# Kernel tuning notes

Measured on AMD Instinct MI355X. Metric: run time of the kernel, lower is better.

The kernel has to match this reference:

```python
import jax, jax.numpy as jnp
import numpy as np

B, S, D, H = 2, 2048, 1024, 16
HD = D // H  # 64


def setup_inputs() -> dict:
    key = jax.random.key(0)
    ks = jax.random.split(key, 10)
    sc = 1.0 / np.sqrt(D)
    return {
        "decoder_hs": jax.random.normal(ks[0], (B, S, D), jnp.float32),
        "encoder_hs": jax.random.normal(ks[1], (B, S, D), jnp.float32),
        "Wq": jax.random.normal(ks[2], (D, D), jnp.float32) * sc,
        "bq": jax.random.normal(ks[3], (D,), jnp.float32) * 0.02,
        "Wk": jax.random.normal(ks[4], (D, D), jnp.float32) * sc,
        "bk": jax.random.normal(ks[5], (D,), jnp.float32) * 0.02,
        "Wv": jax.random.normal(ks[6], (D, D), jnp.float32) * sc,
        "bv": jax.random.normal(ks[7], (D,), jnp.float32) * 0.02,
        "Wp": jax.random.normal(ks[8], (D, D), jnp.float32) * sc,
        "bp": jax.random.normal(ks[9], (D,), jnp.float32) * 0.02,
    }


def reference(decoder_hs, encoder_hs, Wq, bq, Wk, bk, Wv, bv, Wp, bp):
    b, s, d = decoder_hs.shape
    # torch nn.Linear: y = x @ W.T + b, W is [out, in]
    q = decoder_hs @ Wq.T + bq
    k = encoder_hs @ Wk.T + bk
    v = encoder_hs @ Wv.T + bv
    # head split: [b, s, d] -> [b, h, s, hd]
    q = q.reshape(b, s, H, HD).transpose(0, 2, 1, 3)
    k = k.reshape(b, s, H, HD).transpose(0, 2, 1, 3)
    v = v.reshape(b, s, H, HD).transpose(0, 2, 1, 3)
    scale = 1.0 / np.sqrt(HD).astype(np.float32)
    att = jnp.einsum('bhqd,bhkd->bhqk', q, k) * scale
    att = jax.nn.softmax(att, axis=-1)
    y = jnp.einsum('bhqk,bhkd->bhqd', att, v)
    y = y.transpose(0, 2, 1, 3).reshape(b, s, d)
    return y @ Wp.T + bp
```

## Files before the change

kernel.cpp:

```cpp
#include <hip/hip_runtime.h>
#include <hip/hip_bf16.h>
#include <cstdint>
#include <cstddef>

#define BB 2
#define SS 2048
#define DD 1024
#define HH 16
#define HD 64

typedef __attribute__((ext_vector_type(8))) short bf16x8;
typedef __attribute__((ext_vector_type(4))) short bf16x4;
typedef __attribute__((ext_vector_type(4))) float f32x4;

#define MFMA16(va, vb, c) __builtin_amdgcn_mfma_f32_16x16x16bf16_1k(va, vb, c, 0, 0, 0)

#define GLL(g, l) __builtin_amdgcn_global_load_lds( \
    (const __attribute__((address_space(1))) void*)(g), \
    (__attribute__((address_space(3))) void*)(l), 16, 0, 0)

__device__ __forceinline__ short f2bf_fast(float f) {
    uint32_t u = __float_as_uint(f);
    u += 0x7FFF + ((u >> 16) & 1);
    return (short)(u >> 16);
}
__device__ __forceinline__ uint32_t pack_bf2(float a, float b) {
    uint32_t ua = __float_as_uint(a), ub = __float_as_uint(b);
    ua += 0x7FFF + ((ua >> 16) & 1);
    ub += 0x7FFF + ((ub >> 16) & 1);
    return (ua >> 16) | (ub & 0xFFFF0000u);
}
__device__ __forceinline__ bf16x8 cvt8(const float* __restrict__ p) {
    float4 a = *(const float4*)p;
    float4 b = *(const float4*)(p + 4);
    union { uint32_t d[4]; bf16x8 v; } r;
    r.d[0] = pack_bf2(a.x, a.y);
    r.d[1] = pack_bf2(a.z, a.w);
    r.d[2] = pack_bf2(b.x, b.y);
    r.d[3] = pack_bf2(b.z, b.w);
    return r.v;
}

__global__ __launch_bounds__(256) void cvt6_kernel(
    const float* __restrict__ s0, const float* __restrict__ s1,
    const float* __restrict__ s2, const float* __restrict__ s3,
    const float* __restrict__ s4, const float* __restrict__ s5,
    short* __restrict__ d0, short* __restrict__ d1, short* __restrict__ d2,
    short* __restrict__ d3, short* __restrict__ d4, short* __restrict__ d5)
{
    const int z = blockIdx.z;
    const float* s = (z == 0) ? s0 : (z == 1) ? s1 : (z == 2) ? s2
                   : (z == 3) ? s3 : (z == 4) ? s4 : s5;
    short* d = (z == 0) ? d0 : (z == 1) ? d1 : (z == 2) ? d2
             : (z == 3) ? d3 : (z == 4) ? d4 : d5;
    const int n8 = (z < 2) ? (BB * SS * DD / 8) : (DD * DD / 8);
    const int id = blockIdx.x * 256 + threadIdx.x;
    if (id >= n8) return;
    bf16x8 r = cvt8(s + (size_t)id * 8);
    *(uint4*)(d + (size_t)id * 8) = *(uint4*)&r;
}

template<int BF>
__global__ __launch_bounds__(256, 3) void qkv_gemm_kernel(
    const void* __restrict__ dec, const void* __restrict__ enc,
    const void* __restrict__ Wq, const void* __restrict__ Wk,
    const void* __restrict__ Wv,
    const float* __restrict__ bq, const float* __restrict__ bk,
    const float* __restrict__ bv,
    short* __restrict__ Qo, short* __restrict__ Ko, short* __restrict__ Vo)
{
    __shared__ short As[128 * 32];
    __shared__ short Bs[128 * 32];

    const int z = blockIdx.z;
    const void* Xv = (z == 0) ? dec : enc;
    const void* Wp_ = (z == 0) ? Wq : (z == 1) ? Wk : Wv;
    const float* bias = (z == 0) ? bq : (z == 1) ? bk : bv;
    short* Yo = (z == 0) ? Qo : (z == 1) ? Ko : Vo;

    const int t = threadIdx.x;
    const int lane = t & 63, wv = t >> 6;
    const int lr = lane & 15, quad = lane >> 4;
    const int wm = wv >> 1, wn = wv & 1;
    const int m0 = blockIdx.y * 128;
    const int n0 = blockIdx.x * 128;
    const int K = DD;

    f32x4 acc[4][4];
    #pragma unroll
    for (int i = 0; i < 4; i++)
        #pragma unroll
        for (int j = 0; j < 4; j++) acc[i][j] = (f32x4){0.f, 0.f, 0.f, 0.f};

    for (int kb = 0; kb < K; kb += 32) {
        __syncthreads();
        if (BF) {
            const short* Xb = (const short*)Xv;
            const short* Wb = (const short*)Wp_;
            #pragma unroll
            for (int c = 0; c < 2; c++) {
                int r0 = wv * 32 + c * 16;
                int r = r0 + (lane >> 2), ch = (lane & 3) * 8;
                GLL(Xb + (size_t)(m0 + r) * K + kb + ch, &As[r0 * 32]);
                GLL(Wb + (size_t)(n0 + r) * K + kb + ch, &Bs[r0 * 32]);
            }
        } else {
            const float* Xf = (const float*)Xv;
            const float* Wf = (const float*)Wp_;
            #pragma unroll
            for (int c = 0; c < 2; c++) {
                int id = t + c * 256;
                int r = id >> 2, c8 = (id & 3) * 8;
                *(bf16x8*)&As[r * 32 + c8] = cvt8(Xf + (size_t)(m0 + r) * K + kb + c8);
                *(bf16x8*)&Bs[r * 32 + c8] = cvt8(Wf + (size_t)(n0 + r) * K + kb + c8);
            }
        }
        __syncthreads();

        bf16x8 af[4], bfr[4];
        #pragma unroll
        for (int mi = 0; mi < 4; mi++)
            af[mi] = *(const bf16x8*)&As[(wm * 64 + mi * 16 + lr) * 32 + quad * 8];
        #pragma unroll
        for (int ni = 0; ni < 4; ni++)
            bfr[ni] = *(const bf16x8*)&Bs[(wn * 64 + ni * 16 + lr) * 32 + quad * 8];
        #pragma unroll
        for (int mi = 0; mi < 4; mi++)
            #pragma unroll
            for (int ni = 0; ni < 4; ni++)
                acc[mi][ni] = __builtin_amdgcn_mfma_f32_16x16x32_bf16(
                    af[mi], bfr[ni], acc[mi][ni], 0, 0, 0);
    }

    #pragma unroll
    for (int ni = 0; ni < 4; ni++) {
        int col = n0 + wn * 64 + ni * 16 + lr;
        int h = col >> 6, hd = col & 63;
        float bvv = bias[col];
        #pragma unroll
        for (int mi = 0; mi < 4; mi++) {
            #pragma unroll
            for (int r2 = 0; r2 < 4; r2++) {
                int row = m0 + wm * 64 + mi * 16 + quad * 4 + r2;
                int b = row >> 11, s = row & 2047;
                float v = acc[mi][ni][r2] + bvv;
                size_t off;
                if (z < 2)
                    off = ((size_t)(b * HH + h) * SS + s) * HD + hd;
                else
                    off = ((size_t)(b * HH + h) * HD + hd) * SS + s;
                Yo[off] = f2bf_fast(v);
            }
        }
    }
}

template<int WBF>
__global__ __launch_bounds__(256, 2) void proj_gemm_kernel(
    const short* __restrict__ X,
    const void* __restrict__ W, const float* __restrict__ bias,
    float* __restrict__ Y)
{
    __shared__ short As[64 * 32];
    __shared__ short Bs[128 * 32];

    const int t = threadIdx.x;
    const int lane = t & 63, wv = t >> 6;
    const int lr = lane & 15, quad = lane >> 4;
    const int wm = wv >> 1, wn = wv & 1;
    const int m0 = blockIdx.y * 64;
    const int n0 = blockIdx.x * 128;
    const int K = DD, N = DD;

    f32x4 acc[2][4];
    #pragma unroll
    for (int i = 0; i < 2; i++)
        #pragma unroll
        for (int j = 0; j < 4; j++) acc[i][j] = (f32x4){0.f, 0.f, 0.f, 0.f};

    for (int kb = 0; kb < K; kb += 32) {
        __syncthreads();
        {
            int r0 = wv * 16;
            int r = r0 + (lane >> 2), ch = (lane & 3) * 8;
            GLL(X + (size_t)(m0 + r) * K + kb + ch, &As[r0 * 32]);
        }
        if (WBF) {
            const short* Wb = (const short*)W;
            #pragma unroll
            for (int c = 0; c < 2; c++) {
                int r0 = wv * 32 + c * 16;
                int r = r0 + (lane >> 2), ch = (lane & 3) * 8;
                GLL(Wb + (size_t)(n0 + r) * K + kb + ch, &Bs[r0 * 32]);
            }
        } else {
            const float* Wf = (const float*)W;
            #pragma unroll
            for (int c = 0; c < 2; c++) {
                int id = t + c * 256;
                int r = id >> 2, c8 = (id & 3) * 8;
                *(bf16x8*)&Bs[r * 32 + c8] = cvt8(Wf + (size_t)(n0 + r) * K + kb + c8);
            }
        }
        __syncthreads();

        bf16x8 af[2], bfr[4];
        #pragma unroll
        for (int mi = 0; mi < 2; mi++)
            af[mi] = *(const bf16x8*)&As[(wm * 32 + mi * 16 + lr) * 32 + quad * 8];
        #pragma unroll
        for (int ni = 0; ni < 4; ni++)
            bfr[ni] = *(const bf16x8*)&Bs[(wn * 64 + ni * 16 + lr) * 32 + quad * 8];
        #pragma unroll
        for (int mi = 0; mi < 2; mi++)
            #pragma unroll
            for (int ni = 0; ni < 4; ni++)
                acc[mi][ni] = __builtin_amdgcn_mfma_f32_16x16x32_bf16(
                    af[mi], bfr[ni], acc[mi][ni], 0, 0, 0);
    }

    #pragma unroll
    for (int ni = 0; ni < 4; ni++) {
        int col = n0 + wn * 64 + ni * 16 + lr;
        float bvv = bias[col];
        #pragma unroll
        for (int mi = 0; mi < 2; mi++) {
            #pragma unroll
            for (int r2 = 0; r2 < 4; r2++) {
                int row = m0 + wm * 32 + mi * 16 + quad * 4 + r2;
                Y[(size_t)row * N + col] = acc[mi][ni][r2] + bvv;
            }
        }
    }
}

__global__ __launch_bounds__(256, 4) void attn_kernel(
    const short* __restrict__ Q,
    const short* __restrict__ Kgl,
    const short* __restrict__ Vt_g,
    short* __restrict__ Y)
{
    __shared__ short Ks[128][72];
    __shared__ short Vt[64][136];

    const int t = threadIdx.x;
    const int lane = t & 63, w = t >> 6;
    const int lr = lane & 15, quad = lane >> 4;

    const int qt = blockIdx.x & 31;
    const int bh = blockIdx.x >> 5;
    const int b = bh >> 4, h = bh & 15;

    const float C = 0.125f * 1.44269504088896f;

    const short* Qp = Q + ((size_t)bh * SS + qt * 64 + w * 16 + lr) * HD;
    bf16x8 qf0 = *(const bf16x8*)(Qp + quad * 8);
    bf16x8 qf1 = *(const bf16x8*)(Qp + 32 + quad * 8);

    f32x4 o[4];
    #pragma unroll
    for (int i = 0; i < 4; i++) o[i] = (f32x4){0.f, 0.f, 0.f, 0.f};
    float lsum = 0.f;

    const uint4* Kg0 = (const uint4*)(Kgl + (size_t)bh * SS * HD);
    const short* Vg0 = Vt_g + (size_t)bh * HD * SS;

    for (int kt = 0; kt < SS / 128; kt++) {
        __syncthreads();
        const uint4* Kg = Kg0 + (size_t)kt * 128 * 8;
        #pragma unroll
        for (int c = 0; c < 4; c++) {
            int id = t + c * 256;
            int row = id >> 3, h8 = id & 7;
            *(uint4*)&Ks[row][h8 * 8] = Kg[id];
        }
        #pragma unroll
        for (int c = 0; c < 4; c++) {
            int id = t + c * 256;
            int hd = id >> 4, s16 = id & 15;
            *(uint4*)&Vt[hd][s16 * 8] =
                *(const uint4*)(Vg0 + (size_t)hd * SS + kt * 128 + s16 * 8);
        }
        __syncthreads();

        f32x4 sc[8];
        #pragma unroll
        for (int nt = 0; nt < 8; nt++) {
            bf16x8 kf0 = *(const bf16x8*)&Ks[nt * 16 + lr][quad * 8];
            bf16x8 kf1 = *(const bf16x8*)&Ks[nt * 16 + lr][32 + quad * 8];
            sc[nt] = __builtin_amdgcn_mfma_f32_16x16x32_bf16(
                kf0, qf0, (f32x4){0.f, 0.f, 0.f, 0.f}, 0, 0, 0);
            sc[nt] = __builtin_amdgcn_mfma_f32_16x16x32_bf16(kf1, qf1, sc[nt], 0, 0, 0);
        }

        bf16x4 pb[8];
        #pragma unroll
        for (int nt = 0; nt < 8; nt++) {
            float p0 = __builtin_amdgcn_exp2f(sc[nt][0] * C);
            float p1 = __builtin_amdgcn_exp2f(sc[nt][1] * C);
            float p2 = __builtin_amdgcn_exp2f(sc[nt][2] * C);
            float p3 = __builtin_amdgcn_exp2f(sc[nt][3] * C);
            lsum += (p0 + p1) + (p2 + p3);
            union { uint32_t d[2]; bf16x4 v; } u;
            u.d[0] = pack_bf2(p0, p1);
            u.d[1] = pack_bf2(p2, p3);
            pb[nt] = u.v;
        }

        #pragma unroll
        for (int dt = 0; dt < 4; dt++) {
            #pragma unroll
            for (int nt = 0; nt < 8; nt++) {
                bf16x4 va = *(const bf16x4*)&Vt[dt * 16 + lr][nt * 16 + quad * 4];
                o[dt] = MFMA16(va, pb[nt], o[dt]);
            }
        }
    }

    lsum += __shfl_xor(lsum, 16, 64);
    lsum += __shfl_xor(lsum, 32, 64);
    float inv = 1.0f / lsum;

    const int srow = qt * 64 + w * 16 + lr;
    short* Yp = Y + ((size_t)b * SS + srow) * DD + h * 64 + quad * 4;
    #pragma unroll
    for (int dt = 0; dt < 4; dt++) {
        union { uint32_t d[2]; } u;
        u.d[0] = pack_bf2(o[dt][0] * inv, o[dt][1] * inv);
        u.d[1] = pack_bf2(o[dt][2] * inv, o[dt][3] * inv);
        *(uint2*)(Yp + dt * 16) = *(uint2*)&u;
    }
}

extern "C" void kernel_launch(void* const* d_in, const int* in_sizes, int n_in,
                              void* d_out, int out_size, void* d_ws, size_t ws_size,
                              hipStream_t stream) {
    const float* dec = (const float*)d_in[0];
    const float* enc = (const float*)d_in[1];
    const float* Wq  = (const float*)d_in[2];
    const float* bq  = (const float*)d_in[3];
    const float* Wk  = (const float*)d_in[4];
    const float* bk  = (const float*)d_in[5];
    const float* Wv  = (const float*)d_in[6];
    const float* bv  = (const float*)d_in[7];
    const float* Wp  = (const float*)d_in[8];
    const float* bp  = (const float*)d_in[9];

    const size_t per = (size_t)BB * HH * SS * HD;
    const size_t wsz = (size_t)DD * DD;
    short* ws = (short*)d_ws;
    short* Qb  = ws;
    short* Kb  = ws + per;
    short* Vtb = ws + 2 * per;
    short* Yb  = ws + 3 * per;

    dim3 qkv_grid(DD / 128, (BB * SS) / 128, 3);
    dim3 proj_grid(DD / 128, (BB * SS) / 64);
    const int attn_blocks = BB * HH * (SS / 64);

    const size_t need = (6 * per + 4 * wsz) * sizeof(short);
    if (ws_size >= need) {
        short* decb = ws + 4 * per;
        short* encb = ws + 5 * per;
        short* Wqb  = ws + 6 * per;
        short* Wkb  = Wqb + wsz;
        short* Wvb  = Wqb + 2 * wsz;
        short* Wpb  = Wqb + 3 * wsz;
        cvt6_kernel<<<dim3((BB * SS * DD / 8 + 255) / 256, 1, 6), 256, 0, stream>>>(
            dec, enc, Wq, Wk, Wv, Wp, decb, encb, Wqb, Wkb, Wvb, Wpb);
        qkv_gemm_kernel<1><<<qkv_grid, 256, 0, stream>>>(
            decb, encb, Wqb, Wkb, Wvb, bq, bk, bv, Qb, Kb, Vtb);
        attn_kernel<<<attn_blocks, 256, 0, stream>>>(Qb, Kb, Vtb, Yb);
        proj_gemm_kernel<1><<<proj_grid, 256, 0, stream>>>(Yb, Wpb, bp, (float*)d_out);
    } else {
        qkv_gemm_kernel<0><<<qkv_grid, 256, 0, stream>>>(
            dec, enc, Wq, Wk, Wv, bq, bk, bv, Qb, Kb, Vtb);
        attn_kernel<<<attn_blocks, 256, 0, stream>>>(Qb, Kb, Vtb, Yb);
        proj_gemm_kernel<0><<<proj_grid, 256, 0, stream>>>(Yb, Wp, bp, (float*)d_out);
    }
}
```

Baseline: 240.7 us.

## Process two query sub-tiles per wave in attention and vectorize V-transpose stores

```diff
diff --git a/kernel.cpp b/kernel.cpp
--- a/kernel.cpp
+++ b/kernel.cpp
@@ -132,24 +132,39 @@
                     af[mi], bfr[ni], acc[mi][ni], 0, 0, 0);
     }
 
-    #pragma unroll
-    for (int ni = 0; ni < 4; ni++) {
-        int col = n0 + wn * 64 + ni * 16 + lr;
-        int h = col >> 6, hd = col & 63;
-        float bvv = bias[col];
-        #pragma unroll
-        for (int mi = 0; mi < 4; mi++) {
-            #pragma unroll
-            for (int r2 = 0; r2 < 4; r2++) {
-                int row = m0 + wm * 64 + mi * 16 + quad * 4 + r2;
-                int b = row >> 11, s = row & 2047;
-                float v = acc[mi][ni][r2] + bvv;
-                size_t off;
-                if (z < 2)
-                    off = ((size_t)(b * HH + h) * SS + s) * HD + hd;
-                else
-                    off = ((size_t)(b * HH + h) * HD + hd) * SS + s;
-                Yo[off] = f2bf_fast(v);
+    if (z < 2) {
+        #pragma unroll
+        for (int ni = 0; ni < 4; ni++) {
+            int col = n0 + wn * 64 + ni * 16 + lr;
+            int h = col >> 6, hd = col & 63;
+            float bvv = bias[col];
+            #pragma unroll
+            for (int mi = 0; mi < 4; mi++) {
+                #pragma unroll
+                for (int r2 = 0; r2 < 4; r2++) {
+                    int row = m0 + wm * 64 + mi * 16 + quad * 4 + r2;
+                    int b = row >> 11, s = row & 2047;
+                    float v = acc[mi][ni][r2] + bvv;
+                    size_t off = ((size_t)(b * HH + h) * SS + s) * HD + hd;
+                    Yo[off] = f2bf_fast(v);
+                }
+            }
+        }
+    } else {
+        #pragma unroll
+        for (int ni = 0; ni < 4; ni++) {
+            int col = n0 + wn * 64 + ni * 16 + lr;
+            int h = col >> 6, hd = col & 63;
+            float bvv = bias[col];
+            #pragma unroll
+            for (int mi = 0; mi < 4; mi++) {
+                int s0 = m0 + wm * 64 + mi * 16 + quad * 4;
+                int b = s0 >> 11, s = s0 & 2047;
+                union { uint32_t d[2]; } u;
+                u.d[0] = pack_bf2(acc[mi][ni][0] + bvv, acc[mi][ni][1] + bvv);
+                u.d[1] = pack_bf2(acc[mi][ni][2] + bvv, acc[mi][ni][3] + bvv);
+                size_t off = ((size_t)(b * HH + h) * HD + hd) * SS + s;
+                *(uint2*)(Yo + off) = *(uint2*)&u;
             }
         }
     }
@@ -234,7 +249,7 @@
     }
 }
 
-__global__ __launch_bounds__(256, 4) void attn_kernel(
+__global__ __launch_bounds__(256, 2) void attn_kernel(
     const short* __restrict__ Q,
     const short* __restrict__ Kgl,
     const short* __restrict__ Vt_g,
@@ -247,20 +262,26 @@
     const int lane = t & 63, w = t >> 6;
     const int lr = lane & 15, quad = lane >> 4;
 
-    const int qt = blockIdx.x & 31;
-    const int bh = blockIdx.x >> 5;
+    const int qt = blockIdx.x & 15;
+    const int bh = blockIdx.x >> 4;
     const int b = bh >> 4, h = bh & 15;
 
     const float C = 0.125f * 1.44269504088896f;
 
-    const short* Qp = Q + ((size_t)bh * SS + qt * 64 + w * 16 + lr) * HD;
-    bf16x8 qf0 = *(const bf16x8*)(Qp + quad * 8);
-    bf16x8 qf1 = *(const bf16x8*)(Qp + 32 + quad * 8);
-
-    f32x4 o[4];
+    const short* QpA = Q + ((size_t)bh * SS + qt * 128 + w * 32 + lr) * HD;
+    const short* QpB = QpA + 16 * HD;
+    bf16x8 qfA0 = *(const bf16x8*)(QpA + quad * 8);
+    bf16x8 qfA1 = *(const bf16x8*)(QpA + 32 + quad * 8);
+    bf16x8 qfB0 = *(const bf16x8*)(QpB + quad * 8);
+    bf16x8 qfB1 = *(const bf16x8*)(QpB + 32 + quad * 8);
+
+    f32x4 oA[4], oB[4];
     #pragma unroll
-    for (int i = 0; i < 4; i++) o[i] = (f32x4){0.f, 0.f, 0.f, 0.f};
-    float lsum = 0.f;
+    for (int i = 0; i < 4; i++) {
+        oA[i] = (f32x4){0.f, 0.f, 0.f, 0.f};
+        oB[i] = (f32x4){0.f, 0.f, 0.f, 0.f};
+    }
+    float lsumA = 0.f, lsumB = 0.f;
 
     const uint4* Kg0 = (const uint4*)(Kgl + (size_t)bh * SS * HD);
     const short* Vg0 = Vt_g + (size_t)bh * HD * SS;
@@ -283,28 +304,40 @@
         }
         __syncthreads();
 
-        f32x4 sc[8];
+        f32x4 scA[8], scB[8];
         #pragma unroll
         for (int nt = 0; nt < 8; nt++) {
             bf16x8 kf0 = *(const bf16x8*)&Ks[nt * 16 + lr][quad * 8];
             bf16x8 kf1 = *(const bf16x8*)&Ks[nt * 16 + lr][32 + quad * 8];
-            sc[nt] = __builtin_amdgcn_mfma_f32_16x16x32_bf16(
-                kf0, qf0, (f32x4){0.f, 0.f, 0.f, 0.f}, 0, 0, 0);
-            sc[nt] = __builtin_amdgcn_mfma_f32_16x16x32_bf16(kf1, qf1, sc[nt], 0, 0, 0);
-        }
-
-        bf16x4 pb[8];
+            scA[nt] = __builtin_amdgcn_mfma_f32_16x16x32_bf16(
+                kf0, qfA0, (f32x4){0.f, 0.f, 0.f, 0.f}, 0, 0, 0);
+            scA[nt] = __builtin_amdgcn_mfma_f32_16x16x32_bf16(kf1, qfA1, scA[nt], 0, 0, 0);
+            scB[nt] = __builtin_amdgcn_mfma_f32_16x16x32_bf16(
+                kf0, qfB0, (f32x4){0.f, 0.f, 0.f, 0.f}, 0, 0, 0);
+            scB[nt] = __builtin_amdgcn_mfma_f32_16x16x32_bf16(kf1, qfB1, scB[nt], 0, 0, 0);
+        }
+
+        bf16x4 pbA[8], pbB[8];
         #pragma unroll
         for (int nt = 0; nt < 8; nt++) {
-            float p0 = __builtin_amdgcn_exp2f(sc[nt][0] * C);
-            float p1 = __builtin_amdgcn_exp2f(sc[nt][1] * C);
-            float p2 = __builtin_amdgcn_exp2f(sc[nt][2] * C);
-            float p3 = __builtin_amdgcn_exp2f(sc[nt][3] * C);
-            lsum += (p0 + p1) + (p2 + p3);
-            union { uint32_t d[2]; bf16x4 v; } u;
-            u.d[0] = pack_bf2(p0, p1);
-            u.d[1] = pack_bf2(p2, p3);
-            pb[nt] = u.v;
+            float a0 = __builtin_amdgcn_exp2f(scA[nt][0] * C);
+            float a1 = __builtin_amdgcn_exp2f(scA[nt][1] * C);
+            float a2 = __builtin_amdgcn_exp2f(scA[nt][2] * C);
+            float a3 = __builtin_amdgcn_exp2f(scA[nt][3] * C);
+            lsumA += (a0 + a1) + (a2 + a3);
+            union { uint32_t d[2]; bf16x4 v; } ua;
+            ua.d[0] = pack_bf2(a0, a1);
+            ua.d[1] = pack_bf2(a2, a3);
+            pbA[nt] = ua.v;
+            float b0 = __builtin_amdgcn_exp2f(scB[nt][0] * C);
+            float b1 = __builtin_amdgcn_exp2f(scB[nt][1] * C);
+            float b2 = __builtin_amdgcn_exp2f(scB[nt][2] * C);
+            float b3 = __builtin_amdgcn_exp2f(scB[nt][3] * C);
+            lsumB += (b0 + b1) + (b2 + b3);
+            union { uint32_t d[2]; bf16x4 v; } ub;
+            ub.d[0] = pack_bf2(b0, b1);
+            ub.d[1] = pack_bf2(b2, b3);
+            pbB[nt] = ub.v;
         }
 
         #pragma unroll
@@ -312,23 +345,31 @@
             #pragma unroll
             for (int nt = 0; nt < 8; nt++) {
                 bf16x4 va = *(const bf16x4*)&Vt[dt * 16 + lr][nt * 16 + quad * 4];
-                o[dt] = MFMA16(va, pb[nt], o[dt]);
-            }
-        }
-    }
-
-    lsum += __shfl_xor(lsum, 16, 64);
-    lsum += __shfl_xor(lsum, 32, 64);
-    float inv = 1.0f / lsum;
-
-    const int srow = qt * 64 + w * 16 + lr;
-    short* Yp = Y + ((size_t)b * SS + srow) * DD + h * 64 + quad * 4;
+                oA[dt] = MFMA16(va, pbA[nt], oA[dt]);
+                oB[dt] = MFMA16(va, pbB[nt], oB[dt]);
+            }
+        }
+    }
+
+    lsumA += __shfl_xor(lsumA, 16, 64);
+    lsumA += __shfl_xor(lsumA, 32, 64);
+    lsumB += __shfl_xor(lsumB, 16, 64);
+    lsumB += __shfl_xor(lsumB, 32, 64);
+    float invA = 1.0f / lsumA, invB = 1.0f / lsumB;
+
+    const int srowA = qt * 128 + w * 32 + lr;
+    short* YpA = Y + ((size_t)b * SS + srowA) * DD + h * 64 + quad * 4;
+    short* YpB = YpA + 16 * DD;
     #pragma unroll
     for (int dt = 0; dt < 4; dt++) {
-        union { uint32_t d[2]; } u;
-        u.d[0] = pack_bf2(o[dt][0] * inv, o[dt][1] * inv);
-        u.d[1] = pack_bf2(o[dt][2] * inv, o[dt][3] * inv);
-        *(uint2*)(Yp + dt * 16) = *(uint2*)&u;
+        union { uint32_t d[2]; } ua;
+        ua.d[0] = pack_bf2(oA[dt][0] * invA, oA[dt][1] * invA);
+        ua.d[1] = pack_bf2(oA[dt][2] * invA, oA[dt][3] * invA);
+        *(uint2*)(YpA + dt * 16) = *(uint2*)&ua;
+        union { uint32_t d[2]; } ub;
+        ub.d[0] = pack_bf2(oB[dt][0] * invB, oB[dt][1] * invB);
+        ub.d[1] = pack_bf2(oB[dt][2] * invB, oB[dt][3] * invB);
+        *(uint2*)(YpB + dt * 16) = *(uint2*)&ub;
     }
 }
 
@@ -356,7 +397,7 @@
 
     dim3 qkv_grid(DD / 128, (BB * SS) / 128, 3);
     dim3 proj_grid(DD / 128, (BB * SS) / 64);
-    const int attn_blocks = BB * HH * (SS / 64);
+    const int attn_blocks = BB * HH * (SS / 128);
 
     const size_t need = (6 * per + 4 * wsz) * sizeof(short);
     if (ws_size >= need) {
```

After: 215.3 us. -10.5%, faster.
